# Performance work log

Measured on AMD Instinct MI355X. Metric: run time of the kernel, lower is better.

Reference implementation:

```python
import jax, jax.numpy as jnp
import numpy as np

B, K, M, D = 2048, 64, 64, 256
NI, EPS, MI = 15, 0.05, 3


def setup_inputs() -> dict:
    key = jax.random.key(0)
    ks = jax.random.split(key, 8)
    sq = jax.random.normal(ks[0], (B, K, D), dtype=jnp.float32)
    sr = jax.random.normal(ks[1], (B, M, D), dtype=jnp.float32)
    mq = jax.random.uniform(ks[2], (B, K), dtype=jnp.float32)
    mr = jax.random.uniform(ks[3], (B, M), dtype=jnp.float32)
    scale = 1.0 / np.sqrt(D)
    W1 = jax.random.normal(ks[4], (D, D), dtype=jnp.float32) * scale
    b1 = jnp.zeros((D,), dtype=jnp.float32)
    W2 = jax.random.normal(ks[5], (D, D), dtype=jnp.float32) * scale
    b2 = jnp.zeros((D,), dtype=jnp.float32)
    return {"sq": sq, "sr": sr, "mq": mq, "mr": mr,
            "W1": W1, "b1": b1, "W2": W2, "b2": b2}


def _mlp(x, W1, b1, W2, b2):
    # nn.Linear: x @ W.T + b
    h = jax.nn.relu(jnp.einsum('bnd,ed->bne', x, W1) + b1)
    return jnp.einsum('bnd,ed->bne', h, W2) + b2


def _cdist(x, y):
    # Euclidean pairwise distance [B,K,M]
    x2 = jnp.sum(x * x, -1)[:, :, None]
    y2 = jnp.sum(y * y, -1)[:, None, :]
    xy = jnp.einsum('bkd,bmd->bkm', x, y)
    return jnp.sqrt(jnp.clip(x2 + y2 - 2.0 * xy, 0.0))


def reference(sq, sr, mq, mr, W1, b1, W2, b2):
    fq = _mlp(sq, W1, b1, W2, b2)
    fr = _mlp(sr, W1, b1, W2, b2)
    C = _cdist(fq, fr)                                   # [B,K,M]
    lK = (-C / EPS
          + jnp.log(jnp.clip(mq, 1e-8))[:, :, None]
          + jnp.log(jnp.clip(mr, 1e-8))[:, None, :])

    la0 = jnp.zeros((B, K, 1), dtype=C.dtype)
    lb0 = jnp.zeros((B, 1, M), dtype=C.dtype)

    def sink_body(_, carry):
        la, lb = carry
        la = -jax.nn.logsumexp(lK + lb, axis=2, keepdims=True)
        lb = -jax.nn.logsumexp(lK + la, axis=1, keepdims=True)
        return (la, lb)

    la, lb = jax.lax.fori_loop(0, NI, sink_body, (la0, lb0))
    T = jnp.exp(lK + la + lb)

    def pow_body(_, T):
        T = T * T
        T = T / (jnp.sum(T, -1, keepdims=True) + 1e-8)
        T = T / (jnp.sum(T, -2, keepdims=True) + 1e-8)
        return T

    T = jax.lax.fori_loop(0, MI, pow_body, T)
    c = jnp.sum(T * C, axis=(-1, -2))                    # [B]
    return (jax.nn.sigmoid(-c), T, C, c)
```

## Files before the change

kernel.cpp:

```cpp
#include <hip/hip_runtime.h>
#include <math.h>

#define NB    2048
#define KK    64
#define MM    64
#define DD    256
#define NITER 15
#define MITER 3
#define IEPS  20.0f

typedef __bf16 bf16_t;
typedef bf16_t bf16x8 __attribute__((ext_vector_type(8)));
typedef bf16_t bf16x4 __attribute__((ext_vector_type(4)));
typedef float  f32x16 __attribute__((ext_vector_type(16)));

#define XSTR 264
#define CSTR 65


__global__ __launch_bounds__(256) void convert_w_frag(const float* __restrict__ W1,
                                                      const float* __restrict__ W2,
                                                      bf16_t* __restrict__ wf) {
    const int j19 = blockIdx.x * 256 + threadIdx.x;
    const int layer = j19 >> 16;
    const int j = j19 & 65535;
    const int u    = j & 7;
    const int lane = (j >> 3) & 63;
    const int kc   = (j >> 9) & 15;
    const int eb   = j >> 13;
    const int l31  = lane & 31;
    const int lh   = lane >> 5;
    const int src  = (eb * 32 + l31) * 256 + kc * 16 + lh * 8 + u;
    wf[j19] = (bf16_t)(layer ? W2[src] : W1[src]);
}

__global__ __launch_bounds__(512, 4) void mlp_cdist(
    const float* __restrict__ sq, const float* __restrict__ sr,
    const float* __restrict__ b1, const float* __restrict__ b2,
    const bf16_t* __restrict__ wf,
    float* __restrict__ out) {

    __shared__ __align__(16) char smem[128 * XSTR * 2];
    bf16_t* Xs = (bf16_t*)smem;
    __shared__ float nrm[128];
    __shared__ float b1_s[256], b2_s[256];

    const int b  = blockIdx.x;
    const int t  = threadIdx.x;
    const int ln = t & 63;
    const int wv = t >> 6;
    const int l31 = ln & 31;
    const int lh  = ln >> 5;

    {
        const float4* sq4 = (const float4*)(sq + (size_t)b * 64 * 256);
        const float4* sr4 = (const float4*)(sr + (size_t)b * 64 * 256);
        float4 xr[16];
        #pragma unroll
        for (int it = 0; it < 16; ++it) {
            const int r = wv + it * 8;
            xr[it] = (r < 64) ? sq4[r * 64 + ln] : sr4[(r - 64) * 64 + ln];
        }
        #pragma unroll
        for (int it = 0; it < 16; ++it) {
            const int r = wv + it * 8;
            bf16x4 p;
            p[0] = (bf16_t)xr[it].x; p[1] = (bf16_t)xr[it].y;
            p[2] = (bf16_t)xr[it].z; p[3] = (bf16_t)xr[it].w;
            *(bf16x4*)&Xs[(size_t)r * XSTR + ln * 4] = p;
        }
        if (t < 256) b1_s[t] = b1[t];
        else         b2_s[t - 256] = b2[t - 256];
    }
    __syncthreads();

    bf16x4 hreg[2][2][4];
    {
        const bf16_t* wbase = wf + ((size_t)wv * 16) * 512 + ln * 8;
        f32x16 acc[2][2];
        #pragma unroll
        for (int i = 0; i < 16; ++i) {
            acc[0][0][i] = 0.0f; acc[0][1][i] = 0.0f;
            acc[1][0][i] = 0.0f; acc[1][1][i] = 0.0f;
        }
        #pragma unroll
        for (int kg = 0; kg < 2; ++kg) {
            bf16x8 af[8];
            #pragma unroll
            for (int u = 0; u < 8; ++u)
                af[u] = *(const bf16x8*)(wbase + (size_t)(kg * 8 + u) * 512);
            #pragma unroll
            for (int half = 0; half < 2; ++half) {
                const bf16_t* x0 = Xs + (size_t)(half * 64 + l31) * XSTR + lh * 8;
                const bf16_t* x1 = x0 + 32 * XSTR;
                #pragma unroll
                for (int u = 0; u < 8; ++u) {
                    const int kc = kg * 8 + u;
                    bf16x8 bx0 = *(const bf16x8*)(x0 + kc * 16);
                    bf16x8 bx1 = *(const bf16x8*)(x1 + kc * 16);
                    acc[half][0] = __builtin_amdgcn_mfma_f32_32x32x16_bf16(af[u], bx0, acc[half][0], 0, 0, 0);
                    acc[half][1] = __builtin_amdgcn_mfma_f32_32x32x16_bf16(af[u], bx1, acc[half][1], 0, 0, 0);
                }
            }
        }
        const int e0 = wv * 32;
        #pragma unroll
        for (int half = 0; half < 2; ++half)
            #pragma unroll
            for (int z = 0; z < 2; ++z)
                #pragma unroll
                for (int g = 0; g < 4; ++g) {
                    const int e = e0 + 8 * g + 4 * lh;
                    #pragma unroll
                    for (int rr = 0; rr < 4; ++rr) {
                        float v = acc[half][z][4 * g + rr] + b1_s[e + rr];
                        hreg[half][z][g][rr] = (bf16_t)fmaxf(v, 0.0f);
                    }
                }
    }
    __syncthreads();

    {
        const int e0 = wv * 32;
        #pragma unroll
        for (int half = 0; half < 2; ++half)
            #pragma unroll
            for (int z = 0; z < 2; ++z) {
                const int n = half * 64 + z * 32 + l31;
                #pragma unroll
                for (int g = 0; g < 4; ++g)
                    *(bf16x4*)&Xs[(size_t)n * XSTR + e0 + 8 * g + 4 * lh] = hreg[half][z][g];
            }
    }
    __syncthreads();

    {
        const bf16_t* wbase = wf + 65536 + ((size_t)wv * 16) * 512 + ln * 8;
        f32x16 acc[2][2];
        #pragma unroll
        for (int i = 0; i < 16; ++i) {
            acc[0][0][i] = 0.0f; acc[0][1][i] = 0.0f;
            acc[1][0][i] = 0.0f; acc[1][1][i] = 0.0f;
        }
        #pragma unroll
        for (int kg = 0; kg < 2; ++kg) {
            bf16x8 af[8];
            #pragma unroll
            for (int u = 0; u < 8; ++u)
                af[u] = *(const bf16x8*)(wbase + (size_t)(kg * 8 + u) * 512);
            #pragma unroll
            for (int half = 0; half < 2; ++half) {
                const bf16_t* x0 = Xs + (size_t)(half * 64 + l31) * XSTR + lh * 8;
                const bf16_t* x1 = x0 + 32 * XSTR;
                #pragma unroll
                for (int u = 0; u < 8; ++u) {
                    const int kc = kg * 8 + u;
                    bf16x8 bx0 = *(const bf16x8*)(x0 + kc * 16);
                    bf16x8 bx1 = *(const bf16x8*)(x1 + kc * 16);
                    acc[half][0] = __builtin_amdgcn_mfma_f32_32x32x16_bf16(af[u], bx0, acc[half][0], 0, 0, 0);
                    acc[half][1] = __builtin_amdgcn_mfma_f32_32x32x16_bf16(af[u], bx1, acc[half][1], 0, 0, 0);
                }
            }
        }
        const int e0 = wv * 32;
        #pragma unroll
        for (int half = 0; half < 2; ++half)
            #pragma unroll
            for (int z = 0; z < 2; ++z)
                #pragma unroll
                for (int g = 0; g < 4; ++g) {
                    const int e = e0 + 8 * g + 4 * lh;
                    #pragma unroll
                    for (int rr = 0; rr < 4; ++rr)
                        hreg[half][z][g][rr] = (bf16_t)(acc[half][z][4 * g + rr] + b2_s[e + rr]);
                }
    }
    __syncthreads();

    {
        const int e0 = wv * 32;
        #pragma unroll
        for (int half = 0; half < 2; ++half)
            #pragma unroll
            for (int z = 0; z < 2; ++z) {
                const int n = half * 64 + z * 32 + l31;
                #pragma unroll
                for (int g = 0; g < 4; ++g)
                    *(bf16x4*)&Xs[(size_t)n * XSTR + e0 + 8 * g + 4 * lh] = hreg[half][z][g];
            }
    }
    __syncthreads();

    {
        const int r = t >> 2;
        const int q = t & 3;
        const bf16_t* frow = &Xs[(size_t)r * XSTR + q * 64];
        float s = 0.0f;
        #pragma unroll
        for (int c = 0; c < 8; ++c) {
            bf16x8 v = *(const bf16x8*)(frow + c * 8);
            #pragma unroll
            for (int u = 0; u < 8; ++u) { float f = (float)v[u]; s = fmaf(f, f, s); }
        }
        s += __shfl_xor(s, 1);
        s += __shfl_xor(s, 2);
        if (q == 0) nrm[r] = s;
    }
    __syncthreads();

    if (wv < 4) {
        const int qt = wv >> 1, rt = wv & 1;
        const bf16_t* qa = &Xs[(size_t)(qt * 32 + l31) * XSTR + lh * 8];
        const bf16_t* ra = &Xs[(size_t)(64 + rt * 32 + l31) * XSTR + lh * 8];
        f32x16 acc;
        #pragma unroll
        for (int i = 0; i < 16; ++i) acc[i] = 0.0f;
        #pragma unroll
        for (int kc = 0; kc < 16; ++kc) {
            bf16x8 av = *(const bf16x8*)(qa + kc * 16);
            bf16x8 bv = *(const bf16x8*)(ra + kc * 16);
            acc = __builtin_amdgcn_mfma_f32_32x32x16_bf16(av, bv, acc, 0, 0, 0);
        }
        const int mcol  = rt * 32 + l31;
        const int qbase = qt * 32;
        const float nr_m = nrm[64 + mcol];
        float* outC = out + 2048 + (size_t)2048 * 4096 + (size_t)b * 4096;
        #pragma unroll
        for (int g = 0; g < 4; ++g) {
            #pragma unroll
            for (int rr = 0; rr < 4; ++rr) {
                const int q = qbase + 8 * g + 4 * lh + rr;
                float d2 = nrm[q] + nr_m - 2.0f * acc[4 * g + rr];
                outC[q * 64 + mcol] = sqrtf(fmaxf(d2, 0.0f));
            }
        }
    }
}

__global__ __launch_bounds__(512, 8) void sinkhorn_from_C(
    const float* __restrict__ mq, const float* __restrict__ mr,
    float* __restrict__ out) {

    __shared__ float Cs[64 * CSTR];
    __shared__ float Ts[64 * CSTR];
    __shared__ float lmq_s[64], lmr_s[64], la_s[64], lb_s[64];
    __shared__ float red_s[8];

    const int b  = blockIdx.x;
    const int t  = threadIdx.x;
    const int ln = t & 63;
    const int wv = t >> 6;
    const int ki = t >> 3;
    const int jj = t & 7;

    const float* Cg = out + 2048 + (size_t)2048 * 4096 + (size_t)b * 4096 + ki * 64 + jj * 8;
    const float4 c0 = ((const float4*)Cg)[0];
    const float4 c1 = ((const float4*)Cg)[1];

    if (t < 64)        lmq_s[t]       = __logf(fmaxf(mq[(size_t)b * 64 + t], 1e-8f));
    else if (t < 128)  lmr_s[t - 64]  = __logf(fmaxf(mr[(size_t)b * 64 + (t - 64)], 1e-8f));
    else if (t < 192)  lb_s[t - 128]  = 0.0f;

    {
        float* cr = &Cs[ki * CSTR + jj * 8];
        cr[0] = c0.x; cr[1] = c0.y; cr[2] = c0.z; cr[3] = c0.w;
        cr[4] = c1.x; cr[5] = c1.y; cr[6] = c1.z; cr[7] = c1.w;
    }
    __syncthreads();

    float rowV[8], colV[8];
    {
        const float cv[8] = {c0.x, c0.y, c0.z, c0.w, c1.x, c1.y, c1.z, c1.w};
        #pragma unroll
        for (int i = 0; i < 8; ++i)
            rowV[i] = fmaf(cv[i], -IEPS, lmr_s[jj * 8 + i]);
        #pragma unroll
        for (int i = 0; i < 8; ++i)
            colV[i] = fmaf(Cs[(jj * 8 + i) * CSTR + ki], -IEPS, lmq_s[jj * 8 + i]);
    }
    const float lmq_k = lmq_s[ki];
    const float lmr_m = lmr_s[ki];

    for (int it = 0; it < NITER; ++it) {
        float mx = -1e30f;
        #pragma unroll
        for (int i = 0; i < 8; ++i) mx = fmaxf(mx, rowV[i] + lb_s[jj * 8 + i]);
        mx = fmaxf(mx, __shfl_xor(mx, 1));
        mx = fmaxf(mx, __shfl_xor(mx, 2));
        mx = fmaxf(mx, __shfl_xor(mx, 4));
        float s = 0.0f;
        #pragma unroll
        for (int i = 0; i < 8; ++i) s += __expf(rowV[i] + lb_s[jj * 8 + i] - mx);
        s += __shfl_xor(s, 1);
        s += __shfl_xor(s, 2);
        s += __shfl_xor(s, 4);
        if (jj == 0) la_s[ki] = -(lmq_k + mx + __logf(s));
        __syncthreads();

        mx = -1e30f;
        #pragma unroll
        for (int i = 0; i < 8; ++i) mx = fmaxf(mx, colV[i] + la_s[jj * 8 + i]);
        mx = fmaxf(mx, __shfl_xor(mx, 1));
        mx = fmaxf(mx, __shfl_xor(mx, 2));
        mx = fmaxf(mx, __shfl_xor(mx, 4));
        float s2 = 0.0f;
        #pragma unroll
        for (int i = 0; i < 8; ++i) s2 += __expf(colV[i] + la_s[jj * 8 + i] - mx);
        s2 += __shfl_xor(s2, 1);
        s2 += __shfl_xor(s2, 2);
        s2 += __shfl_xor(s2, 4);
        if (jj == 0) lb_s[ki] = -(lmr_m + mx + __logf(s2));
        __syncthreads();
    }

    {
        const float base = lmq_k + la_s[ki];
        #pragma unroll
        for (int i = 0; i < 8; ++i) {
            const int m2 = jj * 8 + i;
            Ts[ki * CSTR + m2] = __expf(rowV[i] + lb_s[m2] + base);
        }
    }
    __syncthreads();

    for (int pi = 0; pi < MITER; ++pi) {
        float vv[8], rs = 0.0f;
        #pragma unroll
        for (int i = 0; i < 8; ++i) {
            float v = Ts[ki * CSTR + jj * 8 + i];
            v = v * v; vv[i] = v; rs += v;
        }
        rs += __shfl_xor(rs, 1); rs += __shfl_xor(rs, 2); rs += __shfl_xor(rs, 4);
        float inv = 1.0f / (rs + 1e-8f);
        #pragma unroll
        for (int i = 0; i < 8; ++i) Ts[ki * CSTR + jj * 8 + i] = vv[i] * inv;
        __syncthreads();

        float cs = 0.0f;
        #pragma unroll
        for (int i = 0; i < 8; ++i) { float v = Ts[(jj * 8 + i) * CSTR + ki]; vv[i] = v; cs += v; }
        cs += __shfl_xor(cs, 1); cs += __shfl_xor(cs, 2); cs += __shfl_xor(cs, 4);
        inv = 1.0f / (cs + 1e-8f);
        #pragma unroll
        for (int i = 0; i < 8; ++i) Ts[(jj * 8 + i) * CSTR + ki] = vv[i] * inv;
        __syncthreads();
    }

    {
        float part = 0.0f;
        float tq[8];
        #pragma unroll
        for (int i = 0; i < 8; ++i) {
            const int m2 = jj * 8 + i;
            float tv = Ts[ki * CSTR + m2];
            tq[i] = tv;
            part = fmaf(tv, Cs[ki * CSTR + m2], part);
        }
        float* outT = out + 2048 + (size_t)b * 4096 + ki * 64 + jj * 8;
        ((float4*)outT)[0] = make_float4(tq[0], tq[1], tq[2], tq[3]);
        ((float4*)outT)[1] = make_float4(tq[4], tq[5], tq[6], tq[7]);
        #pragma unroll
        for (int off = 1; off < 64; off <<= 1) part += __shfl_xor(part, off);
        if (ln == 0) red_s[wv] = part;
    }
    __syncthreads();
    if (t == 0) {
        float c = 0.0f;
        #pragma unroll
        for (int w = 0; w < 8; ++w) c += red_s[w];
        out[2048 + (size_t)2 * 2048 * 4096 + b] = c;
        out[b] = 1.0f / (1.0f + __expf(c));
    }
}

extern "C" void kernel_launch(void* const* d_in, const int* in_sizes, int n_in,
                              void* d_out, int out_size, void* d_ws, size_t ws_size,
                              hipStream_t stream) {
    const float* sq = (const float*)d_in[0];
    const float* sr = (const float*)d_in[1];
    const float* mq = (const float*)d_in[2];
    const float* mr = (const float*)d_in[3];
    const float* W1 = (const float*)d_in[4];
    const float* b1 = (const float*)d_in[5];
    const float* W2 = (const float*)d_in[6];
    const float* b2 = (const float*)d_in[7];

    bf16_t* wf = (bf16_t*)d_ws;

    convert_w_frag<<<512, 256, 0, stream>>>(W1, W2, wf);
    mlp_cdist<<<NB, 512, 0, stream>>>(sq, sr, b1, b2, wf, (float*)d_out);
    sinkhorn_from_C<<<NB, 512, 0, stream>>>(mq, mr, (float*)d_out);
}
```

Baseline: 419.2 us.

## Make MLP-cdist kernel persistent with register prefetch of next batch and swizzled LDS

The mlp_cdist kernel now runs 512 blocks that each loop over 4 batches. Each block prefetches the next batch's sq and sr rows into registers while the current batch's GEMMs run. The padded LDS stride is replaced by an XOR swizzle to avoid bank conflicts, and the row norms are folded into the second-layer epilogue using LDS atomics instead of a separate pass. This hides global load latency and trims a barrier phase. In exchange it holds more registers for the prefetch buffers and launches fewer blocks, which may reduce occupancy.

```diff
diff --git a/kernel.cpp b/kernel.cpp
--- a/kernel.cpp
+++ b/kernel.cpp
@@ -9,12 +9,14 @@
 #define MITER 3
 #define IEPS  20.0f
 
+#define NBLK  512
+#define BPB   4
+
 typedef __bf16 bf16_t;
 typedef bf16_t bf16x8 __attribute__((ext_vector_type(8)));
 typedef bf16_t bf16x4 __attribute__((ext_vector_type(4)));
 typedef float  f32x16 __attribute__((ext_vector_type(16)));
 
-#define XSTR 264
 #define CSTR 65
 
 
@@ -40,200 +42,207 @@
     const bf16_t* __restrict__ wf,
     float* __restrict__ out) {
 
-    __shared__ __align__(16) char smem[128 * XSTR * 2];
-    bf16_t* Xs = (bf16_t*)smem;
+    __shared__ __align__(16) bf16_t Xs[128 * 256];
     __shared__ float nrm[128];
     __shared__ float b1_s[256], b2_s[256];
 
-    const int b  = blockIdx.x;
-    const int t  = threadIdx.x;
-    const int ln = t & 63;
-    const int wv = t >> 6;
+    const int t   = threadIdx.x;
+    const int ln  = t & 63;
+    const int wv  = t >> 6;
     const int l31 = ln & 31;
     const int lh  = ln >> 5;
-
+    const int sw  = l31 & 7;
+
+    if (t < 256) b1_s[t] = b1[t];
+    else         b2_s[t - 256] = b2[t - 256];
+
+    int b = blockIdx.x;
+
+    float4 pf0[8], pf1[8];
     {
-        const float4* sq4 = (const float4*)(sq + (size_t)b * 64 * 256);
-        const float4* sr4 = (const float4*)(sr + (size_t)b * 64 * 256);
-        float4 xr[16];
-        #pragma unroll
-        for (int it = 0; it < 16; ++it) {
-            const int r = wv + it * 8;
-            xr[it] = (r < 64) ? sq4[r * 64 + ln] : sr4[(r - 64) * 64 + ln];
-        }
-        #pragma unroll
-        for (int it = 0; it < 16; ++it) {
-            const int r = wv + it * 8;
-            bf16x4 p;
-            p[0] = (bf16_t)xr[it].x; p[1] = (bf16_t)xr[it].y;
-            p[2] = (bf16_t)xr[it].z; p[3] = (bf16_t)xr[it].w;
-            *(bf16x4*)&Xs[(size_t)r * XSTR + ln * 4] = p;
-        }
-        if (t < 256) b1_s[t] = b1[t];
-        else         b2_s[t - 256] = b2[t - 256];
-    }
-    __syncthreads();
-
-    bf16x4 hreg[2][2][4];
-    {
-        const bf16_t* wbase = wf + ((size_t)wv * 16) * 512 + ln * 8;
-        f32x16 acc[2][2];
-        #pragma unroll
-        for (int i = 0; i < 16; ++i) {
-            acc[0][0][i] = 0.0f; acc[0][1][i] = 0.0f;
-            acc[1][0][i] = 0.0f; acc[1][1][i] = 0.0f;
-        }
-        #pragma unroll
-        for (int kg = 0; kg < 2; ++kg) {
-            bf16x8 af[8];
-            #pragma unroll
-            for (int u = 0; u < 8; ++u)
-                af[u] = *(const bf16x8*)(wbase + (size_t)(kg * 8 + u) * 512);
+        const float4* sq4 = (const float4*)(sq + (size_t)b * 16384);
+        const float4* sr4 = (const float4*)(sr + (size_t)b * 16384);
+        #pragma unroll
+        for (int i = 0; i < 8; ++i) pf0[i] = sq4[(wv + i * 8) * 64 + ln];
+        #pragma unroll
+        for (int i = 0; i < 8; ++i) pf1[i] = sr4[(wv + i * 8) * 64 + ln];
+    }
+
+    for (int it = 0; it < BPB; ++it, b += NBLK) {
+        {
+            const int cw = (((ln >> 1) ^ wv) << 3) + (ln & 1) * 4;
+            #pragma unroll
+            for (int i = 0; i < 8; ++i) {
+                const int r = wv + i * 8;
+                bf16x4 p;
+                p[0] = (bf16_t)pf0[i].x; p[1] = (bf16_t)pf0[i].y;
+                p[2] = (bf16_t)pf0[i].z; p[3] = (bf16_t)pf0[i].w;
+                *(bf16x4*)&Xs[r * 256 + cw] = p;
+                bf16x4 q;
+                q[0] = (bf16_t)pf1[i].x; q[1] = (bf16_t)pf1[i].y;
+                q[2] = (bf16_t)pf1[i].z; q[3] = (bf16_t)pf1[i].w;
+                *(bf16x4*)&Xs[(64 + r) * 256 + cw] = q;
+            }
+            if (t < 128) nrm[t] = 0.0f;
+        }
+        __syncthreads();
+
+        if (it < BPB - 1) {
+            const float4* nq4 = (const float4*)(sq + (size_t)(b + NBLK) * 16384);
+            #pragma unroll
+            for (int i = 0; i < 8; ++i) pf0[i] = nq4[(wv + i * 8) * 64 + ln];
+        }
+
+        bf16x4 hreg[2][2][4];
+        #pragma unroll
+        for (int half = 0; half < 2; ++half) {
+            f32x16 acc0, acc1;
+            #pragma unroll
+            for (int i = 0; i < 16; ++i) { acc0[i] = 0.0f; acc1[i] = 0.0f; }
+            const bf16_t* xrow0 = Xs + (half * 64 + l31) * 256;
+            const bf16_t* xrow1 = xrow0 + 32 * 256;
+            #pragma unroll
+            for (int kg = 0; kg < 4; ++kg) {
+                const bf16_t* wbase = wf + ((size_t)wv * 16 + kg * 4) * 512 + ln * 8;
+                bf16x8 af[4];
+                #pragma unroll
+                for (int u = 0; u < 4; ++u)
+                    af[u] = *(const bf16x8*)(wbase + u * 512);
+                #pragma unroll
+                for (int u = 0; u < 4; ++u) {
+                    const int ch = ((2 * (kg * 4 + u) + lh) ^ sw) << 3;
+                    bf16x8 bx0 = *(const bf16x8*)(xrow0 + ch);
+                    bf16x8 bx1 = *(const bf16x8*)(xrow1 + ch);
+                    acc0 = __builtin_amdgcn_mfma_f32_32x32x16_bf16(af[u], bx0, acc0, 0, 0, 0);
+                    acc1 = __builtin_amdgcn_mfma_f32_32x32x16_bf16(af[u], bx1, acc1, 0, 0, 0);
+                }
+            }
+            const int e0 = wv * 32;
+            #pragma unroll
+            for (int g = 0; g < 4; ++g) {
+                const int e = e0 + 8 * g + 4 * lh;
+                #pragma unroll
+                for (int rr = 0; rr < 4; ++rr) {
+                    hreg[half][0][g][rr] = (bf16_t)fmaxf(acc0[4 * g + rr] + b1_s[e + rr], 0.0f);
+                    hreg[half][1][g][rr] = (bf16_t)fmaxf(acc1[4 * g + rr] + b1_s[e + rr], 0.0f);
+                }
+            }
+        }
+        __syncthreads();
+
+        #pragma unroll
+        for (int half = 0; half < 2; ++half)
+            #pragma unroll
+            for (int z = 0; z < 2; ++z) {
+                const int n = half * 64 + z * 32 + l31;
+                #pragma unroll
+                for (int g = 0; g < 4; ++g) {
+                    const int cc = (((wv * 4 + g) ^ sw) << 3) + 4 * lh;
+                    *(bf16x4*)&Xs[n * 256 + cc] = hreg[half][z][g];
+                }
+            }
+        __syncthreads();
+
+        {
+            float ps[2][2] = {{0.0f, 0.0f}, {0.0f, 0.0f}};
             #pragma unroll
             for (int half = 0; half < 2; ++half) {
-                const bf16_t* x0 = Xs + (size_t)(half * 64 + l31) * XSTR + lh * 8;
-                const bf16_t* x1 = x0 + 32 * XSTR;
-                #pragma unroll
-                for (int u = 0; u < 8; ++u) {
-                    const int kc = kg * 8 + u;
-                    bf16x8 bx0 = *(const bf16x8*)(x0 + kc * 16);
-                    bf16x8 bx1 = *(const bf16x8*)(x1 + kc * 16);
-                    acc[half][0] = __builtin_amdgcn_mfma_f32_32x32x16_bf16(af[u], bx0, acc[half][0], 0, 0, 0);
-                    acc[half][1] = __builtin_amdgcn_mfma_f32_32x32x16_bf16(af[u], bx1, acc[half][1], 0, 0, 0);
-                }
-            }
-        }
-        const int e0 = wv * 32;
-        #pragma unroll
-        for (int half = 0; half < 2; ++half)
-            #pragma unroll
-            for (int z = 0; z < 2; ++z)
+                f32x16 acc0, acc1;
+                #pragma unroll
+                for (int i = 0; i < 16; ++i) { acc0[i] = 0.0f; acc1[i] = 0.0f; }
+                const bf16_t* xrow0 = Xs + (half * 64 + l31) * 256;
+                const bf16_t* xrow1 = xrow0 + 32 * 256;
+                #pragma unroll
+                for (int kg = 0; kg < 4; ++kg) {
+                    const bf16_t* wbase = wf + 65536 + ((size_t)wv * 16 + kg * 4) * 512 + ln * 8;
+                    bf16x8 af[4];
+                    #pragma unroll
+                    for (int u = 0; u < 4; ++u)
+                        af[u] = *(const bf16x8*)(wbase + u * 512);
+                    #pragma unroll
+                    for (int u = 0; u < 4; ++u) {
+                        const int ch = ((2 * (kg * 4 + u) + lh) ^ sw) << 3;
+                        bf16x8 bx0 = *(const bf16x8*)(xrow0 + ch);
+                        bf16x8 bx1 = *(const bf16x8*)(xrow1 + ch);
+                        acc0 = __builtin_amdgcn_mfma_f32_32x32x16_bf16(af[u], bx0, acc0, 0, 0, 0);
+                        acc1 = __builtin_amdgcn_mfma_f32_32x32x16_bf16(af[u], bx1, acc1, 0, 0, 0);
+                    }
+                }
+                const int e0 = wv * 32;
                 #pragma unroll
                 for (int g = 0; g < 4; ++g) {
                     const int e = e0 + 8 * g + 4 * lh;
                     #pragma unroll
                     for (int rr = 0; rr < 4; ++rr) {
-                        float v = acc[half][z][4 * g + rr] + b1_s[e + rr];
-                        hreg[half][z][g][rr] = (bf16_t)fmaxf(v, 0.0f);
+                        bf16_t v0 = (bf16_t)(acc0[4 * g + rr] + b2_s[e + rr]);
+                        bf16_t v1 = (bf16_t)(acc1[4 * g + rr] + b2_s[e + rr]);
+                        hreg[half][0][g][rr] = v0;
+                        hreg[half][1][g][rr] = v1;
+                        float f0 = (float)v0, f1 = (float)v1;
+                        ps[half][0] = fmaf(f0, f0, ps[half][0]);
+                        ps[half][1] = fmaf(f1, f1, ps[half][1]);
                     }
                 }
-    }
-    __syncthreads();
-
-    {
-        const int e0 = wv * 32;
+            }
+            #pragma unroll
+            for (int half = 0; half < 2; ++half)
+                #pragma unroll
+                for (int z = 0; z < 2; ++z) {
+                    float s = ps[half][z];
+                    s += __shfl_xor(s, 32);
+                    if (lh == 0) atomicAdd(&nrm[half * 64 + z * 32 + l31], s);
+                }
+        }
+        __syncthreads();
+
         #pragma unroll
         for (int half = 0; half < 2; ++half)
             #pragma unroll
             for (int z = 0; z < 2; ++z) {
                 const int n = half * 64 + z * 32 + l31;
                 #pragma unroll
-                for (int g = 0; g < 4; ++g)
-                    *(bf16x4*)&Xs[(size_t)n * XSTR + e0 + 8 * g + 4 * lh] = hreg[half][z][g];
-            }
-    }
-    __syncthreads();
-
-    {
-        const bf16_t* wbase = wf + 65536 + ((size_t)wv * 16) * 512 + ln * 8;
-        f32x16 acc[2][2];
-        #pragma unroll
-        for (int i = 0; i < 16; ++i) {
-            acc[0][0][i] = 0.0f; acc[0][1][i] = 0.0f;
-            acc[1][0][i] = 0.0f; acc[1][1][i] = 0.0f;
-        }
-        #pragma unroll
-        for (int kg = 0; kg < 2; ++kg) {
-            bf16x8 af[8];
-            #pragma unroll
-            for (int u = 0; u < 8; ++u)
-                af[u] = *(const bf16x8*)(wbase + (size_t)(kg * 8 + u) * 512);
-            #pragma unroll
-            for (int half = 0; half < 2; ++half) {
-                const bf16_t* x0 = Xs + (size_t)(half * 64 + l31) * XSTR + lh * 8;
-                const bf16_t* x1 = x0 + 32 * XSTR;
-                #pragma unroll
-                for (int u = 0; u < 8; ++u) {
-                    const int kc = kg * 8 + u;
-                    bf16x8 bx0 = *(const bf16x8*)(x0 + kc * 16);
-                    bf16x8 bx1 = *(const bf16x8*)(x1 + kc * 16);
-                    acc[half][0] = __builtin_amdgcn_mfma_f32_32x32x16_bf16(af[u], bx0, acc[half][0], 0, 0, 0);
-                    acc[half][1] = __builtin_amdgcn_mfma_f32_32x32x16_bf16(af[u], bx1, acc[half][1], 0, 0, 0);
-                }
-            }
-        }
-        const int e0 = wv * 32;
-        #pragma unroll
-        for (int half = 0; half < 2; ++half)
-            #pragma unroll
-            for (int z = 0; z < 2; ++z)
-                #pragma unroll
                 for (int g = 0; g < 4; ++g) {
-                    const int e = e0 + 8 * g + 4 * lh;
-                    #pragma unroll
-                    for (int rr = 0; rr < 4; ++rr)
-                        hreg[half][z][g][rr] = (bf16_t)(acc[half][z][4 * g + rr] + b2_s[e + rr]);
-                }
-    }
-    __syncthreads();
-
-    {
-        const int e0 = wv * 32;
-        #pragma unroll
-        for (int half = 0; half < 2; ++half)
-            #pragma unroll
-            for (int z = 0; z < 2; ++z) {
-                const int n = half * 64 + z * 32 + l31;
-                #pragma unroll
-                for (int g = 0; g < 4; ++g)
-                    *(bf16x4*)&Xs[(size_t)n * XSTR + e0 + 8 * g + 4 * lh] = hreg[half][z][g];
-            }
-    }
-    __syncthreads();
-
-    {
-        const int r = t >> 2;
-        const int q = t & 3;
-        const bf16_t* frow = &Xs[(size_t)r * XSTR + q * 64];
-        float s = 0.0f;
-        #pragma unroll
-        for (int c = 0; c < 8; ++c) {
-            bf16x8 v = *(const bf16x8*)(frow + c * 8);
-            #pragma unroll
-            for (int u = 0; u < 8; ++u) { float f = (float)v[u]; s = fmaf(f, f, s); }
-        }
-        s += __shfl_xor(s, 1);
-        s += __shfl_xor(s, 2);
-        if (q == 0) nrm[r] = s;
-    }
-    __syncthreads();
-
-    if (wv < 4) {
-        const int qt = wv >> 1, rt = wv & 1;
-        const bf16_t* qa = &Xs[(size_t)(qt * 32 + l31) * XSTR + lh * 8];
-        const bf16_t* ra = &Xs[(size_t)(64 + rt * 32 + l31) * XSTR + lh * 8];
-        f32x16 acc;
-        #pragma unroll
-        for (int i = 0; i < 16; ++i) acc[i] = 0.0f;
-        #pragma unroll
-        for (int kc = 0; kc < 16; ++kc) {
-            bf16x8 av = *(const bf16x8*)(qa + kc * 16);
-            bf16x8 bv = *(const bf16x8*)(ra + kc * 16);
-            acc = __builtin_amdgcn_mfma_f32_32x32x16_bf16(av, bv, acc, 0, 0, 0);
-        }
-        const int mcol  = rt * 32 + l31;
-        const int qbase = qt * 32;
-        const float nr_m = nrm[64 + mcol];
-        float* outC = out + 2048 + (size_t)2048 * 4096 + (size_t)b * 4096;
-        #pragma unroll
-        for (int g = 0; g < 4; ++g) {
-            #pragma unroll
-            for (int rr = 0; rr < 4; ++rr) {
-                const int q = qbase + 8 * g + 4 * lh + rr;
-                float d2 = nrm[q] + nr_m - 2.0f * acc[4 * g + rr];
-                outC[q * 64 + mcol] = sqrtf(fmaxf(d2, 0.0f));
-            }
-        }
+                    const int cc = (((wv * 4 + g) ^ sw) << 3) + 4 * lh;
+                    *(bf16x4*)&Xs[n * 256 + cc] = hreg[half][z][g];
+                }
+            }
+
+        if (it < BPB - 1) {
+            const float4* nr4 = (const float4*)(sr + (size_t)(b + NBLK) * 16384);
+            #pragma unroll
+            for (int i = 0; i < 8; ++i) pf1[i] = nr4[(wv + i * 8) * 64 + ln];
+        }
+        __syncthreads();
+
+        if (wv < 4) {
+            const int qt = wv >> 1, rt = wv & 1;
+            const bf16_t* qa = Xs + (qt * 32 + l31) * 256;
+            const bf16_t* ra = Xs + (64 + rt * 32 + l31) * 256;
+            f32x16 acc;
+            #pragma unroll
+            for (int i = 0; i < 16; ++i) acc[i] = 0.0f;
+            #pragma unroll
+            for (int kc = 0; kc < 16; ++kc) {
+                const int ch = ((2 * kc + lh) ^ sw) << 3;
+                bf16x8 av = *(const bf16x8*)(qa + ch);
+                bf16x8 bv = *(const bf16x8*)(ra + ch);
+                acc = __builtin_amdgcn_mfma_f32_32x32x16_bf16(av, bv, acc, 0, 0, 0);
+            }
+            const int mcol  = rt * 32 + l31;
+            const int qbase = qt * 32;
+            const float nr_m = nrm[64 + mcol];
+            float* outC = out + 2048 + (size_t)2048 * 4096 + (size_t)b * 4096;
+            #pragma unroll
+            for (int g = 0; g < 4; ++g) {
+                #pragma unroll
+                for (int rr = 0; rr < 4; ++rr) {
+                    const int q = qbase + 8 * g + 4 * lh + rr;
+                    float d2 = nrm[q] + nr_m - 2.0f * acc[4 * g + rr];
+                    outC[q * 64 + mcol] = sqrtf(fmaxf(d2, 0.0f));
+                }
+            }
+        }
+        __syncthreads();
     }
 }
 
@@ -388,6 +397,6 @@
     bf16_t* wf = (bf16_t*)d_ws;
 
     convert_w_frag<<<512, 256, 0, stream>>>(W1, W2, wf);
-    mlp_cdist<<<NB, 512, 0, stream>>>(sq, sr, b1, b2, wf, (float*)d_out);
+    mlp_cdist<<<NBLK, 512, 0, stream>>>(sq, sr, b1, b2, wf, (float*)d_out);
     sinkhorn_from_C<<<NB, 512, 0, stream>>>(mq, mr, (float*)d_out);
 }
```

New measurement: 749.5 us. 78.8% more time.

## Remap Sinkhorn to one wavefront per batch with register-resident rows

Applied to the files above, without the earlier changes.

Replaces the 512-thread-per-batch Sinkhorn kernel with a design where each 64-lane wavefront handles one batch item. Each lane keeps its full row and column of the log-kernel in registers, which removes block-wide __syncthreads and per-iteration shuffle reductions. Column sums in the power iterations use 64x6 cross-lane shuffles, and there are 192+ live floats per lane, so register pressure and spills could limit occupancy. The T output is written through shared memory with a transposed store.

```diff
diff --git a/kernel.cpp b/kernel.cpp
--- a/kernel.cpp
+++ b/kernel.cpp
@@ -15,7 +15,6 @@
 typedef float  f32x16 __attribute__((ext_vector_type(16)));
 
 #define XSTR 264
-#define CSTR 65
 
 
 __global__ __launch_bounds__(256) void convert_w_frag(const float* __restrict__ W1,
@@ -237,139 +236,148 @@
     }
 }
 
-__global__ __launch_bounds__(512, 8) void sinkhorn_from_C(
+__global__ __launch_bounds__(256, 2) void sinkhorn_wave(
     const float* __restrict__ mq, const float* __restrict__ mr,
     float* __restrict__ out) {
 
-    __shared__ float Cs[64 * CSTR];
-    __shared__ float Ts[64 * CSTR];
-    __shared__ float lmq_s[64], lmr_s[64], la_s[64], lb_s[64];
-    __shared__ float red_s[8];
-
-    const int b  = blockIdx.x;
+    __shared__ float Cw4[4][64 * 65];
+    __shared__ float lmr4[4][64];
+    __shared__ float la4[4][64];
+    __shared__ float lb4[4][64];
+
     const int t  = threadIdx.x;
     const int ln = t & 63;
     const int wv = t >> 6;
-    const int ki = t >> 3;
-    const int jj = t & 7;
-
-    const float* Cg = out + 2048 + (size_t)2048 * 4096 + (size_t)b * 4096 + ki * 64 + jj * 8;
-    const float4 c0 = ((const float4*)Cg)[0];
-    const float4 c1 = ((const float4*)Cg)[1];
-
-    if (t < 64)        lmq_s[t]       = __logf(fmaxf(mq[(size_t)b * 64 + t], 1e-8f));
-    else if (t < 128)  lmr_s[t - 64]  = __logf(fmaxf(mr[(size_t)b * 64 + (t - 64)], 1e-8f));
-    else if (t < 192)  lb_s[t - 128]  = 0.0f;
-
-    {
-        float* cr = &Cs[ki * CSTR + jj * 8];
-        cr[0] = c0.x; cr[1] = c0.y; cr[2] = c0.z; cr[3] = c0.w;
-        cr[4] = c1.x; cr[5] = c1.y; cr[6] = c1.z; cr[7] = c1.w;
-    }
-    __syncthreads();
-
-    float rowV[8], colV[8];
-    {
-        const float cv[8] = {c0.x, c0.y, c0.z, c0.w, c1.x, c1.y, c1.z, c1.w};
-        #pragma unroll
-        for (int i = 0; i < 8; ++i)
-            rowV[i] = fmaf(cv[i], -IEPS, lmr_s[jj * 8 + i]);
-        #pragma unroll
-        for (int i = 0; i < 8; ++i)
-            colV[i] = fmaf(Cs[(jj * 8 + i) * CSTR + ki], -IEPS, lmq_s[jj * 8 + i]);
-    }
-    const float lmq_k = lmq_s[ki];
-    const float lmr_m = lmr_s[ki];
-
+    const int b  = blockIdx.x * 4 + wv;
+
+    float* Cw   = Cw4[wv];
+    float* lmrw = lmr4[wv];
+    float* law  = la4[wv];
+    float* lbw  = lb4[wv];
+
+    const float lmq_k = __logf(fmaxf(mq[(size_t)b * 64 + ln], 1e-8f));
+    const float lmr_m = __logf(fmaxf(mr[(size_t)b * 64 + ln], 1e-8f));
+    lmrw[ln] = lmr_m;
+    law[ln]  = lmq_k;
+    lbw[ln]  = 0.0f;
+
+    const float* Cg = out + 2048 + (size_t)2048 * 4096 + (size_t)b * 4096;
+    #pragma unroll
+    for (int i = 0; i < 16; ++i) {
+        const int r  = i * 4 + (ln >> 4);
+        const int c4 = (ln & 15) * 4;
+        const float4 vv = *(const float4*)(Cg + r * 64 + c4);
+        float* dst = &Cw[r * 65 + c4];
+        dst[0] = vv.x; dst[1] = vv.y; dst[2] = vv.z; dst[3] = vv.w;
+    }
+
+    float rV[64], cV[64], v[64];
+    #pragma unroll
+    for (int m = 0; m < 64; ++m)
+        rV[m] = fmaf(Cw[ln * 65 + m], -IEPS, lmrw[m]);
+    #pragma unroll
+    for (int j = 0; j < 64; ++j)
+        cV[j] = fmaf(Cw[j * 65 + ln], -IEPS, law[j]);
+
+    float la_k = 0.0f;
     for (int it = 0; it < NITER; ++it) {
-        float mx = -1e30f;
-        #pragma unroll
-        for (int i = 0; i < 8; ++i) mx = fmaxf(mx, rowV[i] + lb_s[jj * 8 + i]);
-        mx = fmaxf(mx, __shfl_xor(mx, 1));
-        mx = fmaxf(mx, __shfl_xor(mx, 2));
-        mx = fmaxf(mx, __shfl_xor(mx, 4));
-        float s = 0.0f;
-        #pragma unroll
-        for (int i = 0; i < 8; ++i) s += __expf(rowV[i] + lb_s[jj * 8 + i] - mx);
-        s += __shfl_xor(s, 1);
-        s += __shfl_xor(s, 2);
-        s += __shfl_xor(s, 4);
-        if (jj == 0) la_s[ki] = -(lmq_k + mx + __logf(s));
-        __syncthreads();
-
-        mx = -1e30f;
-        #pragma unroll
-        for (int i = 0; i < 8; ++i) mx = fmaxf(mx, colV[i] + la_s[jj * 8 + i]);
-        mx = fmaxf(mx, __shfl_xor(mx, 1));
-        mx = fmaxf(mx, __shfl_xor(mx, 2));
-        mx = fmaxf(mx, __shfl_xor(mx, 4));
-        float s2 = 0.0f;
-        #pragma unroll
-        for (int i = 0; i < 8; ++i) s2 += __expf(colV[i] + la_s[jj * 8 + i] - mx);
-        s2 += __shfl_xor(s2, 1);
-        s2 += __shfl_xor(s2, 2);
-        s2 += __shfl_xor(s2, 4);
-        if (jj == 0) lb_s[ki] = -(lmr_m + mx + __logf(s2));
-        __syncthreads();
-    }
-
-    {
-        const float base = lmq_k + la_s[ki];
-        #pragma unroll
-        for (int i = 0; i < 8; ++i) {
-            const int m2 = jj * 8 + i;
-            Ts[ki * CSTR + m2] = __expf(rowV[i] + lb_s[m2] + base);
-        }
-    }
-    __syncthreads();
+        {
+            float m0 = -1e30f, m1 = -1e30f, m2 = -1e30f, m3 = -1e30f;
+            #pragma unroll
+            for (int m = 0; m < 64; m += 4) {
+                v[m]     = rV[m]     + lbw[m];
+                v[m + 1] = rV[m + 1] + lbw[m + 1];
+                v[m + 2] = rV[m + 2] + lbw[m + 2];
+                v[m + 3] = rV[m + 3] + lbw[m + 3];
+                m0 = fmaxf(m0, v[m]);     m1 = fmaxf(m1, v[m + 1]);
+                m2 = fmaxf(m2, v[m + 2]); m3 = fmaxf(m3, v[m + 3]);
+            }
+            const float mx = fmaxf(fmaxf(m0, m1), fmaxf(m2, m3));
+            float s0 = 0.0f, s1 = 0.0f, s2 = 0.0f, s3 = 0.0f;
+            #pragma unroll
+            for (int m = 0; m < 64; m += 4) {
+                s0 += __expf(v[m] - mx);     s1 += __expf(v[m + 1] - mx);
+                s2 += __expf(v[m + 2] - mx); s3 += __expf(v[m + 3] - mx);
+            }
+            la_k = -(lmq_k + mx + __logf((s0 + s1) + (s2 + s3)));
+            law[ln] = la_k;
+        }
+        {
+            float m0 = -1e30f, m1 = -1e30f, m2 = -1e30f, m3 = -1e30f;
+            #pragma unroll
+            for (int j = 0; j < 64; j += 4) {
+                v[j]     = cV[j]     + law[j];
+                v[j + 1] = cV[j + 1] + law[j + 1];
+                v[j + 2] = cV[j + 2] + law[j + 2];
+                v[j + 3] = cV[j + 3] + law[j + 3];
+                m0 = fmaxf(m0, v[j]);     m1 = fmaxf(m1, v[j + 1]);
+                m2 = fmaxf(m2, v[j + 2]); m3 = fmaxf(m3, v[j + 3]);
+            }
+            const float mx = fmaxf(fmaxf(m0, m1), fmaxf(m2, m3));
+            float s0 = 0.0f, s1 = 0.0f, s2 = 0.0f, s3 = 0.0f;
+            #pragma unroll
+            for (int j = 0; j < 64; j += 4) {
+                s0 += __expf(v[j] - mx);     s1 += __expf(v[j + 1] - mx);
+                s2 += __expf(v[j + 2] - mx); s3 += __expf(v[j + 3] - mx);
+            }
+            const float lb_m = -(lmr_m + mx + __logf((s0 + s1) + (s2 + s3)));
+            lbw[ln] = lb_m;
+        }
+    }
+
+    {
+        const float base = lmq_k + la_k;
+        #pragma unroll
+        for (int m = 0; m < 64; ++m)
+            v[m] = __expf(rV[m] + lbw[m] + base);
+    }
 
     for (int pi = 0; pi < MITER; ++pi) {
-        float vv[8], rs = 0.0f;
-        #pragma unroll
-        for (int i = 0; i < 8; ++i) {
-            float v = Ts[ki * CSTR + jj * 8 + i];
-            v = v * v; vv[i] = v; rs += v;
-        }
-        rs += __shfl_xor(rs, 1); rs += __shfl_xor(rs, 2); rs += __shfl_xor(rs, 4);
-        float inv = 1.0f / (rs + 1e-8f);
-        #pragma unroll
-        for (int i = 0; i < 8; ++i) Ts[ki * CSTR + jj * 8 + i] = vv[i] * inv;
-        __syncthreads();
-
-        float cs = 0.0f;
-        #pragma unroll
-        for (int i = 0; i < 8; ++i) { float v = Ts[(jj * 8 + i) * CSTR + ki]; vv[i] = v; cs += v; }
-        cs += __shfl_xor(cs, 1); cs += __shfl_xor(cs, 2); cs += __shfl_xor(cs, 4);
-        inv = 1.0f / (cs + 1e-8f);
-        #pragma unroll
-        for (int i = 0; i < 8; ++i) Ts[(jj * 8 + i) * CSTR + ki] = vv[i] * inv;
-        __syncthreads();
-    }
-
-    {
-        float part = 0.0f;
-        float tq[8];
-        #pragma unroll
-        for (int i = 0; i < 8; ++i) {
-            const int m2 = jj * 8 + i;
-            float tv = Ts[ki * CSTR + m2];
-            tq[i] = tv;
-            part = fmaf(tv, Cs[ki * CSTR + m2], part);
-        }
-        float* outT = out + 2048 + (size_t)b * 4096 + ki * 64 + jj * 8;
-        ((float4*)outT)[0] = make_float4(tq[0], tq[1], tq[2], tq[3]);
-        ((float4*)outT)[1] = make_float4(tq[4], tq[5], tq[6], tq[7]);
-        #pragma unroll
-        for (int off = 1; off < 64; off <<= 1) part += __shfl_xor(part, off);
-        if (ln == 0) red_s[wv] = part;
-    }
-    __syncthreads();
-    if (t == 0) {
-        float c = 0.0f;
-        #pragma unroll
-        for (int w = 0; w < 8; ++w) c += red_s[w];
-        out[2048 + (size_t)2 * 2048 * 4096 + b] = c;
-        out[b] = 1.0f / (1.0f + __expf(c));
+        float r0 = 0.0f, r1 = 0.0f, r2 = 0.0f, r3 = 0.0f;
+        #pragma unroll
+        for (int m = 0; m < 64; m += 4) {
+            v[m] *= v[m]; v[m + 1] *= v[m + 1];
+            v[m + 2] *= v[m + 2]; v[m + 3] *= v[m + 3];
+            r0 += v[m]; r1 += v[m + 1]; r2 += v[m + 2]; r3 += v[m + 3];
+        }
+        const float rinv = 1.0f / (((r0 + r1) + (r2 + r3)) + 1e-8f);
+        #pragma unroll
+        for (int m = 0; m < 64; ++m) v[m] *= rinv;
+
+        #pragma unroll
+        for (int m = 0; m < 64; ++m) cV[m] = v[m];
+        #pragma unroll
+        for (int off = 1; off < 64; off <<= 1) {
+            #pragma unroll
+            for (int m = 0; m < 64; ++m)
+                cV[m] += __shfl_xor(cV[m], off);
+        }
+        #pragma unroll
+        for (int m = 0; m < 64; ++m) v[m] *= 1.0f / (cV[m] + 1e-8f);
+    }
+
+    float d0 = 0.0f, d1 = 0.0f, d2 = 0.0f, d3 = 0.0f;
+    #pragma unroll
+    for (int m = 0; m < 64; m += 4) {
+        d0 = fmaf(v[m],     Cw[ln * 65 + m],     d0);
+        d1 = fmaf(v[m + 1], Cw[ln * 65 + m + 1], d1);
+        d2 = fmaf(v[m + 2], Cw[ln * 65 + m + 2], d2);
+        d3 = fmaf(v[m + 3], Cw[ln * 65 + m + 3], d3);
+    }
+    float part = (d0 + d1) + (d2 + d3);
+    #pragma unroll
+    for (int off = 1; off < 64; off <<= 1) part += __shfl_xor(part, off);
+
+    #pragma unroll
+    for (int m = 0; m < 64; ++m) Cw[ln * 65 + m] = v[m];
+    float* outT = out + 2048 + (size_t)b * 4096;
+    #pragma unroll
+    for (int r = 0; r < 64; ++r)
+        outT[r * 64 + ln] = Cw[r * 65 + ln];
+
+    if (ln == 0) {
+        out[2048 + (size_t)2 * 2048 * 4096 + b] = part;
+        out[b] = 1.0f / (1.0f + __expf(part));
     }
 }
 
@@ -389,5 +397,5 @@
 
     convert_w_frag<<<512, 256, 0, stream>>>(W1, W2, wf);
     mlp_cdist<<<NB, 512, 0, stream>>>(sq, sr, b1, b2, wf, (float*)d_out);
-    sinkhorn_from_C<<<NB, 512, 0, stream>>>(mq, mr, (float*)d_out);
+    sinkhorn_wave<<<NB / 4, 256, 0, stream>>>(mq, mr, (float*)d_out);
 }
```

Result: no change. 427.3 us (+1.9%).

## Persist MLP blocks over 8 batches with async LDS double-buffered input loads

Applied to the files above, without the earlier changes.

The mlp_cdist kernel now runs 256 persistent blocks, each handling 8 batch items. Layer-1 input arrives in four fp32 chunks through global_load_lds into two XOR-swizzled LDS buffers, so the next chunk or batch loads while MFMAs run. Row norms are accumulated from layer-2 outputs with shared atomics, which removes a separate norm pass. The cost is a much smaller grid (256 blocks for 2048 items, so fewer blocks than there are to saturate occupancy), more LDS per block, per-element bf16 conversion at MFMA time, and extra barriers.

```diff
diff --git a/kernel.cpp b/kernel.cpp
--- a/kernel.cpp
+++ b/kernel.cpp
@@ -2,9 +2,6 @@
 #include <math.h>
 
 #define NB    2048
-#define KK    64
-#define MM    64
-#define DD    256
 #define NITER 15
 #define MITER 3
 #define IEPS  20.0f
@@ -14,7 +11,6 @@
 typedef bf16_t bf16x4 __attribute__((ext_vector_type(4)));
 typedef float  f32x16 __attribute__((ext_vector_type(16)));
 
-#define XSTR 264
 #define CSTR 65
 
 
@@ -34,134 +30,100 @@
     wf[j19] = (bf16_t)(layer ? W2[src] : W1[src]);
 }
 
-__global__ __launch_bounds__(512, 4) void mlp_cdist(
+__global__ __launch_bounds__(512, 2) void mlp_cdist(
     const float* __restrict__ sq, const float* __restrict__ sr,
     const float* __restrict__ b1, const float* __restrict__ b2,
     const bf16_t* __restrict__ wf,
     float* __restrict__ out) {
 
-    __shared__ __align__(16) char smem[128 * XSTR * 2];
-    bf16_t* Xs = (bf16_t*)smem;
+    __shared__ __align__(16) float  Xd[2][128 * 64];
+    __shared__ __align__(16) bf16_t Hf[128 * 256];
+    __shared__ float b1_s[256], b2_s[256];
     __shared__ float nrm[128];
-    __shared__ float b1_s[256], b2_s[256];
-
-    const int b  = blockIdx.x;
-    const int t  = threadIdx.x;
-    const int ln = t & 63;
-    const int wv = t >> 6;
+
+    const int t   = threadIdx.x;
+    const int ln  = t & 63;
+    const int wv  = t >> 6;
     const int l31 = ln & 31;
     const int lh  = ln >> 5;
-
-    {
-        const float4* sq4 = (const float4*)(sq + (size_t)b * 64 * 256);
-        const float4* sr4 = (const float4*)(sr + (size_t)b * 64 * 256);
-        float4 xr[16];
-        #pragma unroll
-        for (int it = 0; it < 16; ++it) {
-            const int r = wv + it * 8;
-            xr[it] = (r < 64) ? sq4[r * 64 + ln] : sr4[(r - 64) * 64 + ln];
-        }
-        #pragma unroll
-        for (int it = 0; it < 16; ++it) {
-            const int r = wv + it * 8;
-            bf16x4 p;
-            p[0] = (bf16_t)xr[it].x; p[1] = (bf16_t)xr[it].y;
-            p[2] = (bf16_t)xr[it].z; p[3] = (bf16_t)xr[it].w;
-            *(bf16x4*)&Xs[(size_t)r * XSTR + ln * 4] = p;
-        }
-        if (t < 256) b1_s[t] = b1[t];
-        else         b2_s[t - 256] = b2[t - 256];
-    }
-    __syncthreads();
-
-    bf16x4 hreg[2][2][4];
-    {
-        const bf16_t* wbase = wf + ((size_t)wv * 16) * 512 + ln * 8;
+    const int sk  = l31 & 15;
+
+    if (t < 256) b1_s[t] = b1[t];
+    else         b2_s[t - 256] = b2[t - 256];
+
+    auto issue_chunk = [&](int b, int c, int slot) {
+        const float* base = (wv < 4) ? sq : sr;
+        #pragma unroll
+        for (int i = 0; i < 4; ++i) {
+            const int R    = wv * 16 + i * 4 + (ln >> 4);
+            const int Radj = (wv < 4) ? R : R - 64;
+            const int u    = ln & 15;
+            const float* g = base + (size_t)b * 16384 + (size_t)Radj * 256
+                           + c * 64 + ((u ^ (R & 15)) << 2);
+            float* l = &Xd[slot][(wv * 4 + i) * 256];
+            __builtin_amdgcn_global_load_lds(
+                (const __attribute__((address_space(1))) void*)g,
+                (__attribute__((address_space(3))) void*)l, 16, 0, 0);
+        }
+    };
+
+    auto l1_chunk = [&](int c, int slot, f32x16 acc[2][2]) {
+        const bf16_t* wb = wf + ((size_t)(wv * 16 + c * 4)) * 512 + ln * 8;
+        bf16x8 af[4];
+        #pragma unroll
+        for (int u = 0; u < 4; ++u) af[u] = *(const bf16x8*)(wb + (size_t)u * 512);
+        const float* Xc = &Xd[slot][0];
+        #pragma unroll
+        for (int half = 0; half < 2; ++half) {
+            const float* x0 = Xc + (half * 64 + l31) * 64;
+            const float* x1 = x0 + 32 * 64;
+            #pragma unroll
+            for (int u = 0; u < 4; ++u) {
+                const int p  = u * 4 + lh * 2;
+                const int o0 = ((p ^ sk) << 2);
+                const int o1 = (((p + 1) ^ sk) << 2);
+                float4 a0 = *(const float4*)(x0 + o0);
+                float4 a1 = *(const float4*)(x0 + o1);
+                float4 c0 = *(const float4*)(x1 + o0);
+                float4 c1 = *(const float4*)(x1 + o1);
+                bf16x8 bx0, bx1;
+                bx0[0]=(bf16_t)a0.x; bx0[1]=(bf16_t)a0.y; bx0[2]=(bf16_t)a0.z; bx0[3]=(bf16_t)a0.w;
+                bx0[4]=(bf16_t)a1.x; bx0[5]=(bf16_t)a1.y; bx0[6]=(bf16_t)a1.z; bx0[7]=(bf16_t)a1.w;
+                bx1[0]=(bf16_t)c0.x; bx1[1]=(bf16_t)c0.y; bx1[2]=(bf16_t)c0.z; bx1[3]=(bf16_t)c0.w;
+                bx1[4]=(bf16_t)c1.x; bx1[5]=(bf16_t)c1.y; bx1[6]=(bf16_t)c1.z; bx1[7]=(bf16_t)c1.w;
+                acc[half][0] = __builtin_amdgcn_mfma_f32_32x32x16_bf16(af[u], bx0, acc[half][0], 0, 0, 0);
+                acc[half][1] = __builtin_amdgcn_mfma_f32_32x32x16_bf16(af[u], bx1, acc[half][1], 0, 0, 0);
+            }
+        }
+    };
+
+    int b = blockIdx.x * 8;
+    issue_chunk(b, 0, 0);
+    issue_chunk(b, 1, 1);
+
+    for (int bi = 0; bi < 8; ++bi, ++b) {
+        __syncthreads();
+        if (t < 128) nrm[t] = 0.0f;
+
         f32x16 acc[2][2];
         #pragma unroll
         for (int i = 0; i < 16; ++i) {
             acc[0][0][i] = 0.0f; acc[0][1][i] = 0.0f;
             acc[1][0][i] = 0.0f; acc[1][1][i] = 0.0f;
         }
-        #pragma unroll
-        for (int kg = 0; kg < 2; ++kg) {
-            bf16x8 af[8];
-            #pragma unroll
-            for (int u = 0; u < 8; ++u)
-                af[u] = *(const bf16x8*)(wbase + (size_t)(kg * 8 + u) * 512);
-            #pragma unroll
-            for (int half = 0; half < 2; ++half) {
-                const bf16_t* x0 = Xs + (size_t)(half * 64 + l31) * XSTR + lh * 8;
-                const bf16_t* x1 = x0 + 32 * XSTR;
-                #pragma unroll
-                for (int u = 0; u < 8; ++u) {
-                    const int kc = kg * 8 + u;
-                    bf16x8 bx0 = *(const bf16x8*)(x0 + kc * 16);
-                    bf16x8 bx1 = *(const bf16x8*)(x1 + kc * 16);
-                    acc[half][0] = __builtin_amdgcn_mfma_f32_32x32x16_bf16(af[u], bx0, acc[half][0], 0, 0, 0);
-                    acc[half][1] = __builtin_amdgcn_mfma_f32_32x32x16_bf16(af[u], bx1, acc[half][1], 0, 0, 0);
-                }
-            }
-        }
-        const int e0 = wv * 32;
-        #pragma unroll
-        for (int half = 0; half < 2; ++half)
-            #pragma unroll
-            for (int z = 0; z < 2; ++z)
-                #pragma unroll
-                for (int g = 0; g < 4; ++g) {
-                    const int e = e0 + 8 * g + 4 * lh;
-                    #pragma unroll
-                    for (int rr = 0; rr < 4; ++rr) {
-                        float v = acc[half][z][4 * g + rr] + b1_s[e + rr];
-                        hreg[half][z][g][rr] = (bf16_t)fmaxf(v, 0.0f);
-                    }
-                }
-    }
-    __syncthreads();
-
-    {
-        const int e0 = wv * 32;
-        #pragma unroll
-        for (int half = 0; half < 2; ++half)
-            #pragma unroll
-            for (int z = 0; z < 2; ++z) {
-                const int n = half * 64 + z * 32 + l31;
-                #pragma unroll
-                for (int g = 0; g < 4; ++g)
-                    *(bf16x4*)&Xs[(size_t)n * XSTR + e0 + 8 * g + 4 * lh] = hreg[half][z][g];
-            }
-    }
-    __syncthreads();
-
-    {
-        const bf16_t* wbase = wf + 65536 + ((size_t)wv * 16) * 512 + ln * 8;
-        f32x16 acc[2][2];
-        #pragma unroll
-        for (int i = 0; i < 16; ++i) {
-            acc[0][0][i] = 0.0f; acc[0][1][i] = 0.0f;
-            acc[1][0][i] = 0.0f; acc[1][1][i] = 0.0f;
-        }
-        #pragma unroll
-        for (int kg = 0; kg < 2; ++kg) {
-            bf16x8 af[8];
-            #pragma unroll
-            for (int u = 0; u < 8; ++u)
-                af[u] = *(const bf16x8*)(wbase + (size_t)(kg * 8 + u) * 512);
-            #pragma unroll
-            for (int half = 0; half < 2; ++half) {
-                const bf16_t* x0 = Xs + (size_t)(half * 64 + l31) * XSTR + lh * 8;
-                const bf16_t* x1 = x0 + 32 * XSTR;
-                #pragma unroll
-                for (int u = 0; u < 8; ++u) {
-                    const int kc = kg * 8 + u;
-                    bf16x8 bx0 = *(const bf16x8*)(x0 + kc * 16);
-                    bf16x8 bx1 = *(const bf16x8*)(x1 + kc * 16);
-                    acc[half][0] = __builtin_amdgcn_mfma_f32_32x32x16_bf16(af[u], bx0, acc[half][0], 0, 0, 0);
-                    acc[half][1] = __builtin_amdgcn_mfma_f32_32x32x16_bf16(af[u], bx1, acc[half][1], 0, 0, 0);
-                }
-            }
-        }
+
+        l1_chunk(0, 0, acc);
+        __syncthreads();
+        issue_chunk(b, 2, 0);
+        l1_chunk(1, 1, acc);
+        __syncthreads();
+        issue_chunk(b, 3, 1);
+        l1_chunk(2, 0, acc);
+        __syncthreads();
+        if (bi < 7) issue_chunk(b + 1, 0, 0);
+        l1_chunk(3, 1, acc);
+
+        bf16x4 hreg[2][2][4];
         const int e0 = wv * 32;
         #pragma unroll
         for (int half = 0; half < 2; ++half)
@@ -172,66 +134,119 @@
                     const int e = e0 + 8 * g + 4 * lh;
                     #pragma unroll
                     for (int rr = 0; rr < 4; ++rr)
-                        hreg[half][z][g][rr] = (bf16_t)(acc[half][z][4 * g + rr] + b2_s[e + rr]);
-                }
-    }
-    __syncthreads();
-
-    {
-        const int e0 = wv * 32;
+                        hreg[half][z][g][rr] =
+                            (bf16_t)fmaxf(acc[half][z][4 * g + rr] + b1_s[e + rr], 0.0f);
+                }
+        __syncthreads();
+
         #pragma unroll
         for (int half = 0; half < 2; ++half)
             #pragma unroll
             for (int z = 0; z < 2; ++z) {
                 const int n = half * 64 + z * 32 + l31;
                 #pragma unroll
-                for (int g = 0; g < 4; ++g)
-                    *(bf16x4*)&Xs[(size_t)n * XSTR + e0 + 8 * g + 4 * lh] = hreg[half][z][g];
-            }
-    }
-    __syncthreads();
-
-    {
-        const int r = t >> 2;
-        const int q = t & 3;
-        const bf16_t* frow = &Xs[(size_t)r * XSTR + q * 64];
-        float s = 0.0f;
-        #pragma unroll
-        for (int c = 0; c < 8; ++c) {
-            bf16x8 v = *(const bf16x8*)(frow + c * 8);
-            #pragma unroll
-            for (int u = 0; u < 8; ++u) { float f = (float)v[u]; s = fmaf(f, f, s); }
-        }
-        s += __shfl_xor(s, 1);
-        s += __shfl_xor(s, 2);
-        if (q == 0) nrm[r] = s;
-    }
-    __syncthreads();
-
-    if (wv < 4) {
-        const int qt = wv >> 1, rt = wv & 1;
-        const bf16_t* qa = &Xs[(size_t)(qt * 32 + l31) * XSTR + lh * 8];
-        const bf16_t* ra = &Xs[(size_t)(64 + rt * 32 + l31) * XSTR + lh * 8];
-        f32x16 acc;
-        #pragma unroll
-        for (int i = 0; i < 16; ++i) acc[i] = 0.0f;
-        #pragma unroll
-        for (int kc = 0; kc < 16; ++kc) {
-            bf16x8 av = *(const bf16x8*)(qa + kc * 16);
-            bf16x8 bv = *(const bf16x8*)(ra + kc * 16);
-            acc = __builtin_amdgcn_mfma_f32_32x32x16_bf16(av, bv, acc, 0, 0, 0);
-        }
-        const int mcol  = rt * 32 + l31;
-        const int qbase = qt * 32;
-        const float nr_m = nrm[64 + mcol];
-        float* outC = out + 2048 + (size_t)2048 * 4096 + (size_t)b * 4096;
-        #pragma unroll
-        for (int g = 0; g < 4; ++g) {
-            #pragma unroll
-            for (int rr = 0; rr < 4; ++rr) {
-                const int q = qbase + 8 * g + 4 * lh + rr;
-                float d2 = nrm[q] + nr_m - 2.0f * acc[4 * g + rr];
-                outC[q * 64 + mcol] = sqrtf(fmaxf(d2, 0.0f));
+                for (int g = 0; g < 4; ++g) {
+                    const int U = (wv * 4 + g) ^ sk;
+                    *(bf16x4*)&Hf[n * 256 + U * 8 + 4 * lh] = hreg[half][z][g];
+                }
+            }
+        __syncthreads();
+
+        {
+            f32x16 acc2[2][2];
+            #pragma unroll
+            for (int i = 0; i < 16; ++i) {
+                acc2[0][0][i] = 0.0f; acc2[0][1][i] = 0.0f;
+                acc2[1][0][i] = 0.0f; acc2[1][1][i] = 0.0f;
+            }
+            #pragma unroll
+            for (int kg = 0; kg < 2; ++kg) {
+                const bf16_t* wb = wf + 65536 + ((size_t)(wv * 16 + kg * 8)) * 512 + ln * 8;
+                bf16x8 af[8];
+                #pragma unroll
+                for (int u = 0; u < 8; ++u) af[u] = *(const bf16x8*)(wb + (size_t)u * 512);
+                #pragma unroll
+                for (int half = 0; half < 2; ++half) {
+                    const bf16_t* h0 = Hf + (half * 64 + l31) * 256;
+                    const bf16_t* h1 = h0 + 32 * 256;
+                    #pragma unroll
+                    for (int u = 0; u < 8; ++u) {
+                        const int kc = kg * 8 + u;
+                        const int pp = (((kc * 2 + lh) ^ sk) << 3);
+                        bf16x8 bx0 = *(const bf16x8*)(h0 + pp);
+                        bf16x8 bx1 = *(const bf16x8*)(h1 + pp);
+                        acc2[half][0] = __builtin_amdgcn_mfma_f32_32x32x16_bf16(af[u], bx0, acc2[half][0], 0, 0, 0);
+                        acc2[half][1] = __builtin_amdgcn_mfma_f32_32x32x16_bf16(af[u], bx1, acc2[half][1], 0, 0, 0);
+                    }
+                }
+            }
+            float ps[2][2] = {{0.0f, 0.0f}, {0.0f, 0.0f}};
+            #pragma unroll
+            for (int half = 0; half < 2; ++half)
+                #pragma unroll
+                for (int z = 0; z < 2; ++z)
+                    #pragma unroll
+                    for (int g = 0; g < 4; ++g) {
+                        const int e = e0 + 8 * g + 4 * lh;
+                        #pragma unroll
+                        for (int rr = 0; rr < 4; ++rr) {
+                            bf16_t bv = (bf16_t)(acc2[half][z][4 * g + rr] + b2_s[e + rr]);
+                            hreg[half][z][g][rr] = bv;
+                            float fv = (float)bv;
+                            ps[half][z] = fmaf(fv, fv, ps[half][z]);
+                        }
+                    }
+            #pragma unroll
+            for (int half = 0; half < 2; ++half)
+                #pragma unroll
+                for (int z = 0; z < 2; ++z) {
+                    float s = ps[half][z];
+                    s += __shfl_xor(s, 32);
+                    if (lh == 0) atomicAdd(&nrm[half * 64 + z * 32 + l31], s);
+                }
+        }
+        __syncthreads();
+
+        #pragma unroll
+        for (int half = 0; half < 2; ++half)
+            #pragma unroll
+            for (int z = 0; z < 2; ++z) {
+                const int n = half * 64 + z * 32 + l31;
+                #pragma unroll
+                for (int g = 0; g < 4; ++g) {
+                    const int U = (wv * 4 + g) ^ sk;
+                    *(bf16x4*)&Hf[n * 256 + U * 8 + 4 * lh] = hreg[half][z][g];
+                }
+            }
+        __syncthreads();
+        if (bi < 7) issue_chunk(b + 1, 1, 1);
+
+        if (wv < 4) {
+            const int qt = wv >> 1, rt = wv & 1;
+            const bf16_t* qa = Hf + (qt * 32 + l31) * 256;
+            const bf16_t* ra = Hf + (64 + rt * 32 + l31) * 256;
+            f32x16 accc;
+            #pragma unroll
+            for (int i = 0; i < 16; ++i) accc[i] = 0.0f;
+            #pragma unroll
+            for (int kc = 0; kc < 16; ++kc) {
+                const int pp = (((kc * 2 + lh) ^ sk) << 3);
+                bf16x8 av = *(const bf16x8*)(qa + pp);
+                bf16x8 bv = *(const bf16x8*)(ra + pp);
+                accc = __builtin_amdgcn_mfma_f32_32x32x16_bf16(av, bv, accc, 0, 0, 0);
+            }
+            const int mcol  = rt * 32 + l31;
+            const int qbase = qt * 32;
+            const float nr_m = nrm[64 + mcol];
+            float* outC = out + 2048 + (size_t)2048 * 4096 + (size_t)b * 4096;
+            #pragma unroll
+            for (int g = 0; g < 4; ++g) {
+                #pragma unroll
+                for (int rr = 0; rr < 4; ++rr) {
+                    const int q = qbase + 8 * g + 4 * lh + rr;
+                    float d2 = nrm[q] + nr_m - 2.0f * accc[4 * g + rr];
+                    outC[q * 64 + mcol] = sqrtf(fmaxf(d2, 0.0f));
+                }
             }
         }
     }
@@ -388,6 +403,6 @@
     bf16_t* wf = (bf16_t*)d_ws;
 
     convert_w_frag<<<512, 256, 0, stream>>>(W1, W2, wf);
-    mlp_cdist<<<NB, 512, 0, stream>>>(sq, sr, b1, b2, wf, (float*)d_out);
+    mlp_cdist<<<256, 512, 0, stream>>>(sq, sr, b1, b2, wf, (float*)d_out);
     sinkhorn_from_C<<<NB, 512, 0, stream>>>(mq, mr, (float*)d_out);
 }
```

Result: slower. 549.9 us (+31.2%).
